# Kernel tuning notes

Measured on AMD Instinct MI355X. Metric: run time of the kernel, lower is better.

Reference implementation:

```python
import jax, jax.numpy as jnp
import numpy as np

ALPHA = 0.2  # LeakyReLU negative slope
NEG_INF = -1e9


def setup_inputs() -> dict:
    key = jax.random.key(0)
    k1, k2, k3, k4 = jax.random.split(key, 4)
    B, N, IN, OUT = 8, 2048, 512, 32
    graph_input = jax.random.normal(k1, (B, N, IN), dtype=jnp.float32)
    adj = jax.random.randint(k2, (B, N, N), 0, 2, dtype=jnp.int32)
    W_fc = jax.random.normal(k3, (OUT, IN), dtype=jnp.float32) * (1.0 / np.sqrt(IN))
    W_attn = jax.random.normal(k4, (1, 2 * OUT), dtype=jnp.float32) * (1.0 / np.sqrt(2 * OUT))
    return {"graph_input": graph_input, "adj": adj, "W_fc": W_fc, "W_attn": W_attn}


def reference(graph_input, adj, W_fc, W_attn):
    # h: [B, N, 32]
    h = jnp.einsum('bni,oi->bno', graph_input, W_fc)
    out_dim = W_fc.shape[0]
    # attn_fc(cat(h_i, h_j)) is separable: a1.h_i + a2.h_j
    a1 = W_attn[0, :out_dim]   # [32]
    a2 = W_attn[0, out_dim:]   # [32]
    f1 = jnp.einsum('bno,o->bn', h, a1)  # [B, N]
    f2 = jnp.einsum('bno,o->bn', h, a2)  # [B, N]
    scores = jax.nn.leaky_relu(f1[:, :, None] + f2[:, None, :], negative_slope=ALPHA)  # [B,N,N]
    scores = jnp.where(adj == 0, NEG_INF, scores)
    attn = jax.nn.softmax(scores, axis=2)
    # NOTE: original multiplies attention with graph_input (not h)
    h_prime = jnp.einsum('bnm,bmi->bni', attn, graph_input)  # [B, N, IN]
    return jax.nn.elu(h_prime)  # concat=True path
```

## Files before the change

### kernel.cpp

```cpp
#include <hip/hip_runtime.h>
#include <hip/hip_bf16.h>

#define BATCH 8
#define NN    2048
#define FIN   512
#define FOUT  32
#define GALPHA 0.2f
#define NROW  128
#define NIT   32

typedef float  f32x4  __attribute__((ext_vector_type(4)));
typedef __bf16 bf16x8 __attribute__((ext_vector_type(8)));
typedef unsigned short u16;
typedef u16 u16x8 __attribute__((ext_vector_type(8)));

static __device__ __forceinline__ u16 f2bf(float f) {
    __hip_bfloat16 h = __float2bfloat16(f);
    union { __hip_bfloat16 h; u16 u; } c; c.h = h; return c.u;
}
static __device__ __forceinline__ float bf2f(u16 u) {
    union { u16 u; __hip_bfloat16 h; } c; c.u = u; return __bfloat162float(c.h);
}

__global__ void k_w12(const float* __restrict__ Wfc,
                      const float* __restrict__ Wat,
                      float* __restrict__ w1, float* __restrict__ w2) {
    int i = threadIdx.x;
    float s1 = 0.f, s2 = 0.f;
    #pragma unroll
    for (int o = 0; o < FOUT; o++) {
        float wv = Wfc[o * FIN + i];
        s1 += wv * Wat[o];
        s2 += wv * Wat[FOUT + o];
    }
    w1[i] = s1; w2[i] = s2;
}

__global__ void k_xtf(const float* __restrict__ x,
                      const float* __restrict__ w1, const float* __restrict__ w2,
                      __hip_bfloat16* __restrict__ xt,
                      float* __restrict__ f1, float* __restrict__ f2) {
    int bx = blockIdx.x;
    int it = bx & 7, mt = (bx >> 3) & 31, b = bx >> 8;
    int m0 = mt * 64, i0 = it * 64;
    __shared__ u16 tile[64][72];
    int tt = threadIdx.x;
    int mm = tt >> 3;
    int ic = (tt & 7) * 8;
    const float* xb = x + ((size_t)b * NN + m0) * FIN + i0;
    const f32x4* w1p = (const f32x4*)(w1 + i0 + ic);
    const f32x4* w2p = (const f32x4*)(w2 + i0 + ic);
    f32x4 wA = w1p[0], wB = w1p[1], wC = w2p[0], wD = w2p[1];
    float p1[2], p2[2];
    #pragma unroll
    for (int h = 0; h < 2; h++) {
        int m = mm + h * 32;
        const f32x4* src = (const f32x4*)(xb + (size_t)m * FIN + ic);
        f32x4 v0 = src[0], v1 = src[1];
        u16x8 pk;
        float s1 = 0.f, s2 = 0.f;
        #pragma unroll
        for (int j = 0; j < 4; j++) {
            pk[j] = f2bf(v0[j]); pk[4 + j] = f2bf(v1[j]);
            s1 += v0[j] * wA[j] + v1[j] * wB[j];
            s2 += v0[j] * wC[j] + v1[j] * wD[j];
        }
        p1[h] = s1; p2[h] = s2;
        *(u16x8*)&tile[m][ic] = pk;
    }
    #pragma unroll
    for (int off = 1; off < 8; off <<= 1) {
        p1[0] += __shfl_xor(p1[0], off); p1[1] += __shfl_xor(p1[1], off);
        p2[0] += __shfl_xor(p2[0], off); p2[1] += __shfl_xor(p2[1], off);
    }
    if ((tt & 7) == 0) {
        size_t r0 = (size_t)b * NN + m0 + mm;
        atomicAdd(&f1[r0], p1[0]);      atomicAdd(&f1[r0 + 32], p1[1]);
        atomicAdd(&f2[r0], p2[0]);      atomicAdd(&f2[r0 + 32], p2[1]);
    }
    __syncthreads();
    __hip_bfloat16* xtb = xt + ((size_t)b * FIN + i0) * NN + m0;
    int mc = (tt & 7) * 8;
    #pragma unroll
    for (int h = 0; h < 2; h++) {
        int ii = (tt >> 3) + h * 32;
        u16x8 v;
        #pragma unroll
        for (int j = 0; j < 8; j++) v[j] = tile[mc + j][ii];
        *(u16x8*)(xtb + (size_t)ii * NN + mc) = v;
    }
}

__global__ void k_pack(const int* __restrict__ adj, unsigned int* __restrict__ bits) {
    int row  = blockIdx.x * 4 + (threadIdx.x >> 6);
    int lane = threadIdx.x & 63;
    const int* p = adj + (size_t)row * NN + lane * 32;
    unsigned int bv = 0;
    #pragma unroll
    for (int j = 0; j < 8; j++) {
        int4 v = *(const int4*)(p + j * 4);
        bv |= (v.x != 0 ? 1u : 0u) << (j * 4 + 0);
        bv |= (v.y != 0 ? 1u : 0u) << (j * 4 + 1);
        bv |= (v.z != 0 ? 1u : 0u) << (j * 4 + 2);
        bv |= (v.w != 0 ? 1u : 0u) << (j * 4 + 3);
    }
    bits[(size_t)row * 64 + lane] = bv;
}

__global__ __launch_bounds__(512, 2) void k_main(
    const unsigned int* __restrict__ bits, const __hip_bfloat16* __restrict__ xt,
    const float* __restrict__ f1, const float* __restrict__ f2,
    float* __restrict__ out)
{
    const int bx = blockIdx.x;
    const int b = bx & 7, rt = (bx >> 3) & 15, it = bx >> 7;
    const int n0 = rt * NROW;
    const int i0 = it * 256;
    const int tid = threadIdx.x;
    const int lane = tid & 63, wv = tid >> 6;
    const int quad = lane >> 4, l15 = lane & 15;

    __shared__ u16 At[2][NROW * 64];
    __shared__ float rs[NROW];

    const int grow = tid >> 2;
    const int q4   = tid & 3;
    const unsigned short* bp = (const unsigned short*)bits
                               + ((size_t)(b * NN) + n0 + grow) * 128 + q4;
    const float* f2p = f2 + b * NN + q4 * 16;
    const float  f1v = f1[b * NN + n0 + grow];
    const int swz = grow & 7;
    u16* wp0 = &At[0][grow * 64 + (((q4 * 2) ^ swz) * 8)];
    u16* wp1 = &At[0][grow * 64 + (((q4 * 2 + 1) ^ swz) * 8)];
    float rpart = 0.f;

    const __hip_bfloat16* xtp = xt + ((size_t)(b * FIN) + i0 + wv * 32 + l15) * NN + quad * 8;

    f32x4 acc[8][2];
    #pragma unroll
    for (int s = 0; s < 8; s++) { acc[s][0] = (f32x4){0,0,0,0}; acc[s][1] = (f32x4){0,0,0,0}; }

    auto gen = [&](int buf, unsigned int bv, const f32x4* fr) {
        u16x8 pk0, pk1;
        #pragma unroll
        for (int e = 0; e < 16; e++) {
            float s  = f1v + fr[e >> 2][e & 3];
            float ls = fmaxf(s, GALPHA * s);
            float ev = ((bv >> e) & 1u) ? __expf(ls) : 0.f;
            u16 hb = f2bf(ev);
            rpart += bf2f(hb);
            if (e < 8) pk0[e] = hb; else pk1[e - 8] = hb;
        }
        *(u16x8*)(wp0 + buf * (NROW * 64)) = pk0;
        *(u16x8*)(wp1 + buf * (NROW * 64)) = pk1;
    };

    {
        unsigned int b0 = bp[0];
        f32x4 g0[4];
        #pragma unroll
        for (int j = 0; j < 4; j++) g0[j] = *(const f32x4*)(f2p + j * 4);
        gen(0, b0, g0);
    }
    unsigned int brng[2];
    f32x4 frng[2][4];
    brng[1] = bp[4];
    #pragma unroll
    for (int j = 0; j < 4; j++) frng[1][j] = *(const f32x4*)(f2p + 64 + j * 4);
    brng[0] = bp[8];
    #pragma unroll
    for (int j = 0; j < 4; j++) frng[0][j] = *(const f32x4*)(f2p + 128 + j * 4);

    bf16x8 Bc[2][2], Bn[2][2];
    #pragma unroll
    for (int ks = 0; ks < 2; ks++)
        #pragma unroll
        for (int c = 0; c < 2; c++)
            Bc[ks][c] = *(const bf16x8*)(xtp + ks * 32 + (size_t)(c * 16) * NN);
    __syncthreads();

    #pragma unroll 2
    for (int t = 0; t < NIT; t++) {
        const int cur = t & 1;
        if (t < NIT - 1) {
            const __hip_bfloat16* xk = xtp + (t + 1) * 64;
            #pragma unroll
            for (int ks = 0; ks < 2; ks++)
                #pragma unroll
                for (int c = 0; c < 2; c++)
                    Bn[ks][c] = *(const bf16x8*)(xk + ks * 32 + (size_t)(c * 16) * NN);
        }
        #pragma unroll
        for (int ks = 0; ks < 2; ks++) {
            #pragma unroll
            for (int s = 0; s < 8; s++) {
                const int row = s * 16 + l15;
                bf16x8 Af = *(const bf16x8*)&At[cur][row * 64 + (((ks * 4 + quad) ^ (row & 7)) * 8)];
                acc[s][0] = __builtin_amdgcn_mfma_f32_16x16x32_bf16(Af, Bc[ks][0], acc[s][0], 0, 0, 0);
                acc[s][1] = __builtin_amdgcn_mfma_f32_16x16x32_bf16(Af, Bc[ks][1], acc[s][1], 0, 0, 0);
            }
        }
        if (t < NIT - 1) {
            gen(1 - cur, brng[(t + 1) & 1], frng[(t + 1) & 1]);
            if (t < NIT - 2) {
                brng[t & 1] = bp[(t + 2) * 4];
                #pragma unroll
                for (int j = 0; j < 4; j++)
                    frng[t & 1][j] = *(const f32x4*)(f2p + (t + 2) * 64 + j * 4);
            }
        }
        asm volatile("s_waitcnt lgkmcnt(0)\ns_barrier" ::: "memory");
        #pragma unroll
        for (int ks = 0; ks < 2; ks++) {
            Bc[ks][0] = Bn[ks][0]; Bc[ks][1] = Bn[ks][1];
        }
    }

    rpart += __shfl_xor(rpart, 1);
    rpart += __shfl_xor(rpart, 2);
    if (q4 == 0) rs[grow] = 1.0f / rpart;
    __syncthreads();

    #pragma unroll
    for (int s = 0; s < 8; s++) {
        #pragma unroll
        for (int r = 0; r < 4; r++) {
            const int row = s * 16 + quad * 4 + r;
            const float inv = rs[row];
            float* op = out + ((size_t)b * NN + (n0 + row)) * FIN + i0 + wv * 32 + l15;
            #pragma unroll
            for (int c = 0; c < 2; c++) {
                float v = acc[s][c][r] * inv;
                v = v > 0.f ? v : (__expf(v) - 1.f);
                op[c * 16] = v;
            }
        }
    }
}

extern "C" void kernel_launch(void* const* d_in, const int* in_sizes, int n_in,
                              void* d_out, int out_size, void* d_ws, size_t ws_size,
                              hipStream_t stream) {
    const float* x   = (const float*)d_in[0];
    const int*   adj = (const int*)d_in[1];
    const float* Wfc = (const float*)d_in[2];
    const float* Wat = (const float*)d_in[3];
    float* out = (float*)d_out;

    float* w1 = (float*)d_ws;
    float* w2 = w1 + 512;
    float* f1 = w2 + 512;
    float* f2 = f1 + BATCH * NN;
    unsigned int* bits = (unsigned int*)(f2 + BATCH * NN);
    __hip_bfloat16* xt = (__hip_bfloat16*)(bits + (size_t)BATCH * NN * 64);

    hipMemsetAsync(f1, 0, (size_t)2 * BATCH * NN * sizeof(float), stream);
    hipLaunchKernelGGL(k_w12,  dim3(1),    dim3(512), 0, stream, Wfc, Wat, w1, w2);
    hipLaunchKernelGGL(k_xtf,  dim3(2048), dim3(256), 0, stream, x, w1, w2, xt, f1, f2);
    hipLaunchKernelGGL(k_pack, dim3(4096), dim3(256), 0, stream, adj, bits);
    hipLaunchKernelGGL(k_main, dim3(256),  dim3(512), 0, stream, bits, xt, f1, f2, out);
}
```

Before: 284.7 us.

## Fuse prep kernels into one launch and drop memset and atomics

Merges the weight-fold, transpose/projection and adjacency-packing kernels into a single kernel whose block index selects the role. Each transpose block now loops over all 512 input features, so f1/f2 are written directly instead of accumulated with atomics, which also removes the memset. Every projection block recomputes the folded w1/w2 vectors from W_fc into shared memory. This removes three launches and a memset but adds redundant weight-fold work and gives the 256 transpose blocks much more serial work each.

```diff
diff --git a/kernel.cpp b/kernel.cpp
--- a/kernel.cpp
+++ b/kernel.cpp
@@ -22,52 +22,96 @@
     union { u16 u; __hip_bfloat16 h; } c; c.u = u; return __bfloat162float(c.h);
 }
 
-__global__ void k_w12(const float* __restrict__ Wfc,
-                      const float* __restrict__ Wat,
-                      float* __restrict__ w1, float* __restrict__ w2) {
-    int i = threadIdx.x;
-    float s1 = 0.f, s2 = 0.f;
-    #pragma unroll
-    for (int o = 0; o < FOUT; o++) {
-        float wv = Wfc[o * FIN + i];
-        s1 += wv * Wat[o];
-        s2 += wv * Wat[FOUT + o];
-    }
-    w1[i] = s1; w2[i] = s2;
-}
-
-__global__ void k_xtf(const float* __restrict__ x,
-                      const float* __restrict__ w1, const float* __restrict__ w2,
-                      __hip_bfloat16* __restrict__ xt,
-                      float* __restrict__ f1, float* __restrict__ f2) {
-    int bx = blockIdx.x;
-    int it = bx & 7, mt = (bx >> 3) & 31, b = bx >> 8;
-    int m0 = mt * 64, i0 = it * 64;
+__global__ __launch_bounds__(256) void k_prep(
+    const float* __restrict__ x, const int* __restrict__ adj,
+    const float* __restrict__ Wfc, const float* __restrict__ Wat,
+    __hip_bfloat16* __restrict__ xt,
+    float* __restrict__ f1, float* __restrict__ f2,
+    unsigned int* __restrict__ bits)
+{
+    const int bx = blockIdx.x;
+    const int tt = threadIdx.x;
+
+    if (bx >= 256) {
+        int row  = (bx - 256) * 4 + (tt >> 6);
+        int lane = tt & 63;
+        const int* p = adj + (size_t)row * NN + lane * 32;
+        unsigned int bv = 0;
+        #pragma unroll
+        for (int j = 0; j < 8; j++) {
+            int4 v = *(const int4*)(p + j * 4);
+            bv |= (v.x != 0 ? 1u : 0u) << (j * 4 + 0);
+            bv |= (v.y != 0 ? 1u : 0u) << (j * 4 + 1);
+            bv |= (v.z != 0 ? 1u : 0u) << (j * 4 + 2);
+            bv |= (v.w != 0 ? 1u : 0u) << (j * 4 + 3);
+        }
+        bits[(size_t)row * 64 + lane] = bv;
+        return;
+    }
+
     __shared__ u16 tile[64][72];
-    int tt = threadIdx.x;
-    int mm = tt >> 3;
-    int ic = (tt & 7) * 8;
-    const float* xb = x + ((size_t)b * NN + m0) * FIN + i0;
-    const f32x4* w1p = (const f32x4*)(w1 + i0 + ic);
-    const f32x4* w2p = (const f32x4*)(w2 + i0 + ic);
-    f32x4 wA = w1p[0], wB = w1p[1], wC = w2p[0], wD = w2p[1];
-    float p1[2], p2[2];
+    __shared__ __align__(16) float w1s[FIN];
+    __shared__ __align__(16) float w2s[FIN];
+
+    const int b  = bx >> 5;
+    const int mt = bx & 31;
+    const int m0 = mt * 64;
+
     #pragma unroll
     for (int h = 0; h < 2; h++) {
-        int m = mm + h * 32;
-        const f32x4* src = (const f32x4*)(xb + (size_t)m * FIN + ic);
-        f32x4 v0 = src[0], v1 = src[1];
-        u16x8 pk;
+        int i = tt + h * 256;
         float s1 = 0.f, s2 = 0.f;
         #pragma unroll
-        for (int j = 0; j < 4; j++) {
-            pk[j] = f2bf(v0[j]); pk[4 + j] = f2bf(v1[j]);
-            s1 += v0[j] * wA[j] + v1[j] * wB[j];
-            s2 += v0[j] * wC[j] + v1[j] * wD[j];
-        }
-        p1[h] = s1; p2[h] = s2;
-        *(u16x8*)&tile[m][ic] = pk;
-    }
+        for (int o = 0; o < FOUT; o++) {
+            float wv = Wfc[o * FIN + i];
+            s1 += wv * Wat[o];
+            s2 += wv * Wat[FOUT + o];
+        }
+        w1s[i] = s1; w2s[i] = s2;
+    }
+    __syncthreads();
+
+    const int mm  = tt >> 3;
+    const int icl = (tt & 7) * 8;
+    const float* xb = x + ((size_t)b * NN + m0) * FIN;
+    float p1[2] = {0.f, 0.f}, p2[2] = {0.f, 0.f};
+
+    for (int it = 0; it < 8; it++) {
+        const int i0 = it * 64;
+        f32x4 wA = *(const f32x4*)&w1s[i0 + icl];
+        f32x4 wB = *(const f32x4*)&w1s[i0 + icl + 4];
+        f32x4 wC = *(const f32x4*)&w2s[i0 + icl];
+        f32x4 wD = *(const f32x4*)&w2s[i0 + icl + 4];
+        #pragma unroll
+        for (int h = 0; h < 2; h++) {
+            int m = mm + h * 32;
+            const f32x4* src = (const f32x4*)(xb + (size_t)m * FIN + i0 + icl);
+            f32x4 v0 = src[0], v1 = src[1];
+            u16x8 pk;
+            float s1 = 0.f, s2 = 0.f;
+            #pragma unroll
+            for (int j = 0; j < 4; j++) {
+                pk[j] = f2bf(v0[j]); pk[4 + j] = f2bf(v1[j]);
+                s1 += v0[j] * wA[j] + v1[j] * wB[j];
+                s2 += v0[j] * wC[j] + v1[j] * wD[j];
+            }
+            p1[h] += s1; p2[h] += s2;
+            *(u16x8*)&tile[m][icl] = pk;
+        }
+        __syncthreads();
+        __hip_bfloat16* xtb = xt + ((size_t)b * FIN + i0) * NN + m0;
+        const int mc = (tt & 7) * 8;
+        #pragma unroll
+        for (int h = 0; h < 2; h++) {
+            int ii = (tt >> 3) + h * 32;
+            u16x8 v;
+            #pragma unroll
+            for (int j = 0; j < 8; j++) v[j] = tile[mc + j][ii];
+            *(u16x8*)(xtb + (size_t)ii * NN + mc) = v;
+        }
+        if (it < 7) __syncthreads();
+    }
+
     #pragma unroll
     for (int off = 1; off < 8; off <<= 1) {
         p1[0] += __shfl_xor(p1[0], off); p1[1] += __shfl_xor(p1[1], off);
@@ -75,36 +119,9 @@
     }
     if ((tt & 7) == 0) {
         size_t r0 = (size_t)b * NN + m0 + mm;
-        atomicAdd(&f1[r0], p1[0]);      atomicAdd(&f1[r0 + 32], p1[1]);
-        atomicAdd(&f2[r0], p2[0]);      atomicAdd(&f2[r0 + 32], p2[1]);
-    }
-    __syncthreads();
-    __hip_bfloat16* xtb = xt + ((size_t)b * FIN + i0) * NN + m0;
-    int mc = (tt & 7) * 8;
-    #pragma unroll
-    for (int h = 0; h < 2; h++) {
-        int ii = (tt >> 3) + h * 32;
-        u16x8 v;
-        #pragma unroll
-        for (int j = 0; j < 8; j++) v[j] = tile[mc + j][ii];
-        *(u16x8*)(xtb + (size_t)ii * NN + mc) = v;
-    }
-}
-
-__global__ void k_pack(const int* __restrict__ adj, unsigned int* __restrict__ bits) {
-    int row  = blockIdx.x * 4 + (threadIdx.x >> 6);
-    int lane = threadIdx.x & 63;
-    const int* p = adj + (size_t)row * NN + lane * 32;
-    unsigned int bv = 0;
-    #pragma unroll
-    for (int j = 0; j < 8; j++) {
-        int4 v = *(const int4*)(p + j * 4);
-        bv |= (v.x != 0 ? 1u : 0u) << (j * 4 + 0);
-        bv |= (v.y != 0 ? 1u : 0u) << (j * 4 + 1);
-        bv |= (v.z != 0 ? 1u : 0u) << (j * 4 + 2);
-        bv |= (v.w != 0 ? 1u : 0u) << (j * 4 + 3);
-    }
-    bits[(size_t)row * 64 + lane] = bv;
+        f1[r0] = p1[0];      f1[r0 + 32] = p1[1];
+        f2[r0] = p2[0];      f2[r0 + 32] = p2[1];
+    }
 }
 
 __global__ __launch_bounds__(512, 2) void k_main(
@@ -247,16 +264,13 @@
     const float* Wat = (const float*)d_in[3];
     float* out = (float*)d_out;
 
-    float* w1 = (float*)d_ws;
-    float* w2 = w1 + 512;
-    float* f1 = w2 + 512;
+    float* f1 = (float*)d_ws;
     float* f2 = f1 + BATCH * NN;
     unsigned int* bits = (unsigned int*)(f2 + BATCH * NN);
     __hip_bfloat16* xt = (__hip_bfloat16*)(bits + (size_t)BATCH * NN * 64);
 
-    hipMemsetAsync(f1, 0, (size_t)2 * BATCH * NN * sizeof(float), stream);
-    hipLaunchKernelGGL(k_w12,  dim3(1),    dim3(512), 0, stream, Wfc, Wat, w1, w2);
-    hipLaunchKernelGGL(k_xtf,  dim3(2048), dim3(256), 0, stream, x, w1, w2, xt, f1, f2);
-    hipLaunchKernelGGL(k_pack, dim3(4096), dim3(256), 0, stream, adj, bits);
-    hipLaunchKernelGGL(k_main, dim3(256),  dim3(512), 0, stream, bits, xt, f1, f2, out);
-}
+    hipLaunchKernelGGL(k_prep, dim3(4352), dim3(256), 0, stream,
+                       x, adj, Wfc, Wat, xt, f1, f2, bits);
+    hipLaunchKernelGGL(k_main, dim3(256),  dim3(512), 0, stream,
+                       bits, xt, f1, f2, out);
+}
```

After: 294.7 us. +3.5%, slower.
